# Performance work log

Hardware: AMD Instinct MI355X
Metric: run time of the kernel (lower is better)

Reference implementation:

```python
import jax, jax.numpy as jnp
import numpy as np
from jax import lax

NUM_CLASSES = 2
PATCH_NUM = 4
TEMP = 0.5
THRESHOLD = 0.6
BDP, FDP = 0.1, 0.9
W_CONTR, W_ENT, W_CONS = 0.1, 0.01, 1.0
RAMP = 40
EPOCH_SEMI = 5
IGNORE = 255


def conv(x, w, stride):
    return lax.conv_general_dilated(x, w, (stride, stride), 'SAME',
                                    dimension_numbers=('NCHW', 'OIHW', 'NCHW'))


def extractor(x, W1, W2, W3):
    h = jax.nn.relu(conv(x, W1, 2))
    h = jax.nn.relu(conv(h, W2, 2))
    return jax.nn.relu(conv(h, W3, 2))  # stride-8 features [B,256,H/8,W/8]


def resize_bilinear_ac(x, oh, ow):
    # bilinear, align_corners=True (matches F.interpolate(..., align_corners=True))
    B, C, H, W = x.shape
    ys = jnp.linspace(0.0, H - 1.0, oh)
    xs = jnp.linspace(0.0, W - 1.0, ow)
    y0 = jnp.floor(ys).astype(jnp.int32); x0 = jnp.floor(xs).astype(jnp.int32)
    y1 = jnp.minimum(y0 + 1, H - 1);      x1 = jnp.minimum(x0 + 1, W - 1)
    wy = (ys - y0)[:, None].astype(x.dtype)
    wx = (xs - x0)[None, :].astype(x.dtype)
    v00 = x[:, :, y0[:, None], x0[None, :]]
    v01 = x[:, :, y0[:, None], x1[None, :]]
    v10 = x[:, :, y1[:, None], x0[None, :]]
    v11 = x[:, :, y1[:, None], x1[None, :]]
    top = v00 * (1 - wx) + v01 * wx
    bot = v10 * (1 - wx) + v11 * wx
    return top * (1 - wy) + bot * wy


def ce_loss(logits, labels, extra_mask=None):
    # logits [B,C,H,W], labels [B,H,W]; mean over valid pixels
    logp = jax.nn.log_softmax(logits, axis=1)
    safe = jnp.clip(labels, 0, logits.shape[1] - 1)
    nll = -jnp.take_along_axis(logp, safe[:, None], axis=1)[:, 0]
    valid = labels != IGNORE
    if extra_mask is not None:
        valid = valid & extra_mask
    valid = valid.astype(logits.dtype)
    return (nll * valid).sum() / jnp.maximum(valid.sum(), 1.0)


def reference(x_l, y_l, x_ul, epoch, proj_ul_ema, z_ul_ema, W1, W2, W3, Wc, bc, Wp):
    # ---- supervised branch ----
    fea_l = extractor(x_l, W1, W2, W3)
    zl_small = conv(fea_l, Wc, 1) + bc[None, :, None, None]
    z_l = resize_bilinear_ac(zl_small, x_l.shape[2], x_l.shape[3])
    loss_sup = ce_loss(z_l, y_l)
    if epoch < EPOCH_SEMI:
        return loss_sup

    # ---- unsupervised branch ----
    fea_ul = extractor(x_ul, W1, W2, W3)
    proj_ul = conv(fea_ul, Wp, 1)
    proj_ul = proj_ul / jnp.maximum(
        jnp.linalg.norm(proj_ul, axis=1, keepdims=True), 1e-12)
    z_ul = conv(fea_ul, Wc, 1) + bc[None, :, None, None]

    # entropy minimization
    logp_ul = jax.nn.log_softmax(z_ul, axis=1)
    p_ul = jnp.exp(logp_ul)
    loss_ent = (-(p_ul * logp_ul).sum(axis=1)).mean()

    pseudo_label = jnp.argmax(z_ul, axis=1)
    p_ema = jax.nn.softmax(z_ul_ema, axis=1)
    max_probs_ema = p_ema.max(axis=1)
    pseudo_label_ema = jnp.argmax(z_ul_ema, axis=1)
    mask_confident = max_probs_ema > THRESHOLD
    loss_cons = ce_loss(z_ul, pseudo_label_ema, mask_confident)

    # ---- vectorized patch extraction (replaces python loops) ----
    B, C, Hp, Wp_ = proj_ul.shape
    P = PATCH_NUM
    h, w = Hp // P, Wp_ // P

    def to_patches(t):  # [B,C,Hp,Wp] -> [P*P*B, h*w, C], torch loop order (j,k,ii)
        return t.reshape(B, C, P, h, P, w).transpose(2, 4, 0, 3, 5, 1).reshape(P * P * B, h * w, C)

    def lab_patches(l):  # [B,Hp,Wp] -> [P*P*B, h*w]
        return l.reshape(B, P, h, P, w).transpose(1, 3, 0, 2, 4).reshape(P * P * B, h * w)

    pat_s = to_patches(proj_ul)
    pat_e = to_patches(proj_ul_ema)
    lab_s = lab_patches(pseudo_label)
    lab_e = lab_patches(pseudo_label_ema)

    feat_all = jnp.concatenate([pat_s.reshape(-1, C), pat_e.reshape(-1, C)], axis=0)  # [M,C]
    lab_all = jnp.concatenate([lab_s.reshape(-1), lab_e.reshape(-1)], axis=0)

    fc = lab_s.astype(proj_ul.dtype).mean(axis=1)  # foreground fraction per patch
    include = jnp.logical_not((fc > BDP) & (fc < FDP)).astype(proj_ul.dtype)

    def patch_loss(anchors, labels_i):  # anchors [hw,C]
        logits = (anchors @ feat_all.T) / TEMP        # [hw, M]
        logp = jax.nn.log_softmax(logits, axis=-1)
        pos = (labels_i[:, None] == lab_all[None, :]).astype(logits.dtype)
        per_anchor = -(pos * logp).sum(-1) / jnp.maximum(pos.sum(-1), 1.0)
        return per_anchor.mean()

    losses = jax.vmap(patch_loss)(pat_s, lab_s)       # [P*P*B]
    loss_contr = (losses * include).sum() / jnp.maximum(include.sum(), 1.0)

    ramp = min(max(epoch / RAMP, 0.0), 1.0)
    cons_w = W_CONS * float(np.exp(-5.0 * (1.0 - ramp) ** 2))

    loss_tot = loss_sup + W_CONTR * loss_contr + cons_w * loss_cons + W_ENT * loss_ent
    return loss_tot


def setup_inputs() -> dict:
    key = jax.random.key(0)
    ks = jax.random.split(key, 12)
    s = 0.05
    return {
        'x_l': jax.random.normal(ks[0], (4, 3, 320, 320), jnp.float32),
        'y_l': jax.random.randint(ks[1], (4, 320, 320), 0, NUM_CLASSES),
        'x_ul': jax.random.normal(ks[2], (4, 3, 320, 320), jnp.float32),
        'epoch': 10,
        'proj_ul_ema': jax.random.normal(ks[3], (4, 128, 40, 40), jnp.float32),
        'z_ul_ema': jax.random.normal(ks[4], (4, 2, 40, 40), jnp.float32),
        'W1': jax.random.normal(ks[5], (64, 3, 3, 3), jnp.float32) * s,
        'W2': jax.random.normal(ks[6], (128, 64, 3, 3), jnp.float32) * s,
        'W3': jax.random.normal(ks[7], (256, 128, 3, 3), jnp.float32) * s,
        'Wc': jax.random.normal(ks[8], (NUM_CLASSES, 256, 1, 1), jnp.float32) * s,
        'bc': jnp.zeros((NUM_CLASSES,), jnp.float32),
        'Wp': jax.random.normal(ks[9], (128, 256, 1, 1), jnp.float32) * s,
    }
```

## Files before the change

kernel.cpp:

```cpp
#include <hip/hip_runtime.h>
#include <math.h>

typedef unsigned short u16;
typedef __attribute__((ext_vector_type(8))) short bf16x8;
typedef __attribute__((ext_vector_type(4))) float f32x4;

static const size_t WS_FEA1B = 0;
static const size_t WS_FEA2B = 6553600;
static const size_t WS_FEA3  = 9830400;
static const size_t WS_ZLS   = 13107200;
static const size_t WS_ZUL   = 13120000;
static const size_t WS_FEATB = 13132800;
static const size_t WS_LAB   = 13952000;
static const size_t WS_PART  = 13964800;
static const size_t WS_ACC   = 14194176;
static const size_t WS_FC    = 14194192;
static const size_t WS_CSUM  = 14194256;
static const size_t WS_WT2   = 14194512;
static const size_t WS_WT3   = 14231376;
static const size_t WS_WPT   = 14378832;

#define NJS 25

__device__ inline u16 f2bf(float x) {
    unsigned int u = __float_as_uint(x);
    unsigned int r = u + 0x7fffu + ((u >> 16) & 1u);
    return (u16)(r >> 16);
}

__global__ __launch_bounds__(256) void wtrans(
    const float* __restrict__ W2, const float* __restrict__ W3,
    const float* __restrict__ Wp,
    u16* __restrict__ wt2, u16* __restrict__ wt3, u16* __restrict__ wpt)
{
    int tid = blockIdx.x * 256 + threadIdx.x;
    if (tid < 73728) {
        int ci = tid & 63, rest = tid >> 6;
        int co = rest & 127, tap = rest >> 7;
        wt2[tid] = f2bf(W2[((size_t)co*64 + ci)*9 + tap]);
    } else if (tid < 368640) {
        int t3 = tid - 73728;
        int ci = t3 & 127, rest = t3 >> 7;
        int co = rest & 255, tap = rest >> 8;
        wt3[t3] = f2bf(W3[((size_t)co*128 + ci)*9 + tap]);
    } else {
        int tp = tid - 368640;
        wpt[tp] = f2bf(Wp[tp]);
    }
}

__global__ __launch_bounds__(256) void conv1_k(
    const float* __restrict__ x_l, const float* __restrict__ x_ul,
    const float* __restrict__ W1, u16* __restrict__ fea1b)
{
    int oy = blockIdx.x;
    int n  = blockIdx.y;
    const float* x = (n < 4) ? x_l + (size_t)n*307200
                             : x_ul + (size_t)(n-4)*307200;
    int t = threadIdx.x;
    int co = t & 63, g = t >> 6;
    __shared__ float lds[9*324];
    for (int u = t; u < 9*322; u += 256) {
        int plane = u / 322, col = u - plane*322;
        int ci = plane / 3, ky = plane - ci*3;
        int iy = oy*2 + ky;
        float v = 0.f;
        if (iy < 320 && col < 320)
            v = x[((size_t)ci*320 + iy)*320 + col];
        lds[plane*324 + col] = v;
    }
    __syncthreads();
    float w[27];
    #pragma unroll
    for (int k = 0; k < 27; ++k) w[k] = W1[co*27 + k];
    float acc[40];
    #pragma unroll
    for (int i = 0; i < 40; ++i) acc[i] = 0.f;
    #pragma unroll
    for (int ci = 0; ci < 3; ++ci) {
        #pragma unroll
        for (int ky = 0; ky < 3; ++ky) {
            const float* base = &lds[(ci*3+ky)*324 + g*80];
            const float* wk = &w[(ci*3+ky)*3];
            #pragma unroll
            for (int q = 0; q < 10; ++q) {
                float4 a = *(const float4*)&base[q*8];
                float4 b = *(const float4*)&base[q*8+4];
                float2 c = *(const float2*)&base[q*8+8];
                float xx[10] = {a.x,a.y,a.z,a.w,b.x,b.y,b.z,b.w,c.x,c.y};
                #pragma unroll
                for (int oo = 0; oo < 4; ++oo)
                    acc[q*4+oo] += wk[0]*xx[2*oo] + wk[1]*xx[2*oo+1] + wk[2]*xx[2*oo+2];
            }
        }
    }
    u16* dst = fea1b + (((size_t)n*160 + oy)*160 + g*40)*64 + co;
    #pragma unroll
    for (int i = 0; i < 40; ++i)
        dst[(size_t)i*64] = f2bf(fmaxf(acc[i], 0.f));
}

template<int Ci, int Co, int H, int OH, int COG, bool OB>
__global__ __launch_bounds__(256) void conv3x3_nhwc(
    const u16* __restrict__ inb, const u16* __restrict__ wt,
    u16* __restrict__ outb, float* __restrict__ outf)
{
    constexpr int TILES = OH/8;
    int tile = blockIdx.x;
    int co0  = blockIdx.y * (64*COG);
    int n    = blockIdx.z;
    int ty = tile / TILES, tx = tile - ty*TILES;
    int oy0 = ty*8, ox0 = tx*8;
    int iy0 = oy0*2, ix0 = ox0*2;
    int t = threadIdx.x, lane = t & 63, wv = t >> 6;
    int idx15 = lane & 15, kg = lane >> 4;

    __shared__ u16 lds[306*40];

    f32x4 acc[COG][4];
    #pragma unroll
    for (int cog = 0; cog < COG; ++cog)
        #pragma unroll
        for (int nt = 0; nt < 4; ++nt) acc[cog][nt] = (f32x4){0.f,0.f,0.f,0.f};

    int goff[5], loff[5];
    #pragma unroll
    for (int i = 0; i < 5; ++i) {
        int u = t + i*256;
        if (u < 1224) {
            int pix = u >> 2, q = u & 3;
            int iyl = pix / 18, j = pix - iyl*18;
            int iy = iy0 + iyl, ix = ix0 + j;
            bool ok = (iy < H && ix < H);
            goff[i] = ok ? (((n*H + iy)*H + ix)*Ci + q*8) : -1;
            int jp = (j & 1)*9 + (j >> 1);
            loff[i] = (iyl*18 + jp)*40 + q*8;
        } else goff[i] = -2;
    }
    uint4 vreg[5];
    #pragma unroll
    for (int i = 0; i < 5; ++i) {
        if (goff[i] == -2) continue;
        vreg[i] = (goff[i] >= 0) ? *(const uint4*)&inb[(size_t)goff[i]]
                                 : make_uint4(0,0,0,0);
    }

    for (int c0 = 0; c0 < Ci; c0 += 32) {
        __syncthreads();
        #pragma unroll
        for (int i = 0; i < 5; ++i)
            if (goff[i] != -2) *(uint4*)&lds[loff[i]] = vreg[i];
        __syncthreads();
        if (c0 + 32 < Ci) {
            #pragma unroll
            for (int i = 0; i < 5; ++i) {
                if (goff[i] == -2) continue;
                vreg[i] = (goff[i] >= 0) ? *(const uint4*)&inb[(size_t)goff[i] + c0 + 32]
                                         : make_uint4(0,0,0,0);
            }
        }

        bf16x8 A[COG][9];
        #pragma unroll
        for (int cog = 0; cog < COG; ++cog) {
            const u16* wb = wt + (size_t)(co0 + cog*64 + wv*16 + idx15)*Ci + c0 + kg*8;
            #pragma unroll
            for (int tap = 0; tap < 9; ++tap)
                A[cog][tap] = *(const bf16x8*)(wb + (size_t)tap*Co*Ci);
        }

        #pragma unroll
        for (int tap = 0; tap < 9; ++tap) {
            int ky = tap/3, kx = tap - ky*3;
            #pragma unroll
            for (int nt = 0; nt < 4; ++nt) {
                int l = nt*16 + idx15;
                int iyl = 2*(l>>3) + ky;
                int j = 2*(l&7) + kx;
                int jp = (j&1)*9 + (j>>1);
                bf16x8 B = *(const bf16x8*)&lds[(size_t)(iyl*18 + jp)*40 + kg*8];
                #pragma unroll
                for (int cog = 0; cog < COG; ++cog)
                    acc[cog][nt] = __builtin_amdgcn_mfma_f32_16x16x32_bf16(A[cog][tap], B, acc[cog][nt], 0, 0, 0);
            }
        }
    }

    #pragma unroll
    for (int cog = 0; cog < COG; ++cog) {
        int co = co0 + cog*64 + wv*16 + kg*4;
        #pragma unroll
        for (int nt = 0; nt < 4; ++nt) {
            int l = nt*16 + idx15;
            int oy = oy0 + (l>>3), ox = ox0 + (l&7);
            if (OB) {
                u16* dst = outb + (((size_t)n*OH + oy)*OH + ox)*Co + co;
                unsigned int p0 = (unsigned int)f2bf(fmaxf(acc[cog][nt][0],0.f))
                                | ((unsigned int)f2bf(fmaxf(acc[cog][nt][1],0.f)) << 16);
                unsigned int p1 = (unsigned int)f2bf(fmaxf(acc[cog][nt][2],0.f))
                                | ((unsigned int)f2bf(fmaxf(acc[cog][nt][3],0.f)) << 16);
                *(uint2*)dst = make_uint2(p0, p1);
            } else {
                #pragma unroll
                for (int r = 0; r < 4; ++r)
                    outf[(((size_t)n*Co + co + r)*OH + oy)*OH + ox] = fmaxf(acc[cog][nt][r], 0.f);
            }
        }
    }
}

__global__ __launch_bounds__(256) void conv1x1_cls(
    const float* __restrict__ fea, const float* __restrict__ Wc,
    float* __restrict__ z)
{
    int idx = blockIdx.x * 256 + threadIdx.x;
    int cc0 = blockIdx.y * 32;
    int n = idx / 1600, r = idx - n*1600;
    const float* f = fea + ((size_t)n*256 + cc0)*1600 + r;
    float a0 = 0.f, a1 = 0.f;
    #pragma unroll
    for (int ci = 0; ci < 32; ++ci) {
        float v = f[(size_t)ci*1600];
        a0 += v * Wc[cc0+ci];
        a1 += v * Wc[256+cc0+ci];
    }
    atomicAdd(&z[(size_t)n*3200 + r], a0);
    atomicAdd(&z[(size_t)n*3200 + 1600 + r], a1);
}

__global__ __launch_bounds__(256) void loss_sup_kernel(
    const float* __restrict__ zs, const int* __restrict__ y,
    const float* __restrict__ bc, float* __restrict__ acc)
{
    const float step = 39.0f / 319.0f;
    float b0 = bc[0], b1 = bc[1];
    float vn = 0.f, vd = 0.f;
    for (int idx = blockIdx.x*256 + threadIdx.x; idx < 409600; idx += gridDim.x*256) {
        int n  = idx / 102400;
        int r  = idx - n*102400;
        int oy = r / 320, ox = r - oy*320;
        float ty = (float)oy * step, tx = (float)ox * step;
        int y0 = (int)ty, x0 = (int)tx;
        int y1 = min(y0 + 1, 39), x1 = min(x0 + 1, 39);
        float wy = ty - (float)y0, wx = tx - (float)x0;
        const float* base = zs + (size_t)n * 3200;
        float z[2];
        #pragma unroll
        for (int c = 0; c < 2; ++c) {
            const float* pl = base + c * 1600;
            float v00 = pl[y0*40 + x0], v01 = pl[y0*40 + x1];
            float v10 = pl[y1*40 + x0], v11 = pl[y1*40 + x1];
            float top = v00 * (1.f - wx) + v01 * wx;
            float bot = v10 * (1.f - wx) + v11 * wx;
            z[c] = top * (1.f - wy) + bot * wy + (c ? b1 : b0);
        }
        int lab = y[idx];
        bool valid = (lab != 255);
        int sl = min(max(lab, 0), 1);
        float mz  = fmaxf(z[0], z[1]);
        float lse = mz + logf(expf(z[0]-mz) + expf(z[1]-mz));
        float nll = lse - z[sl];
        if (valid) { vn += nll; vd += 1.f; }
    }
    #pragma unroll
    for (int off = 32; off; off >>= 1) { vn += __shfl_down(vn, off); vd += __shfl_down(vd, off); }
    __shared__ float rb[8];
    int wv = threadIdx.x >> 6;
    if ((threadIdx.x & 63) == 0) { rb[wv*2] = vn; rb[wv*2+1] = vd; }
    __syncthreads();
    if (threadIdx.x == 0) {
        atomicAdd(&acc[0], rb[0]+rb[2]+rb[4]+rb[6]);
        atomicAdd(&acc[1], rb[1]+rb[3]+rb[5]+rb[7]);
    }
}

__global__ __launch_bounds__(256) void ul_small_kernel(
    const float* __restrict__ z_ul, const float* __restrict__ z_ema,
    const float* __restrict__ bc,
    int* __restrict__ lab_all, float* __restrict__ acc, float* __restrict__ fc_cnt)
{
    int idx = blockIdx.x * 256 + threadIdx.x;
    int n = idx / 1600;
    int r = idx - n*1600;
    int yy = r / 40, xx = r - yy*40;
    float z0 = z_ul[(size_t)n*3200 + r] + bc[0];
    float z1 = z_ul[(size_t)n*3200 + 1600 + r] + bc[1];
    float m = fmaxf(z0, z1);
    float e0 = expf(z0 - m), e1 = expf(z1 - m);
    float lse = m + logf(e0 + e1);
    float lp0 = z0 - lse, lp1 = z1 - lse;
    float p0 = expf(lp0), p1 = expf(lp1);
    float ent = -(p0*lp0 + p1*lp1);
    int pl = (z1 > z0) ? 1 : 0;
    float ze0 = z_ema[(size_t)n*3200 + r], ze1 = z_ema[(size_t)n*3200 + 1600 + r];
    float me = fmaxf(ze0, ze1);
    float f0 = expf(ze0 - me), f1 = expf(ze1 - me);
    float maxp = 1.f / (f0 + f1);
    int ple = (ze1 > ze0) ? 1 : 0;
    bool mask = (maxp > 0.6f);
    float nll = lse - (ple ? z1 : z0);

    int pi = yy / 10, hi = yy % 10, pj = xx / 10, wi = xx % 10;
    int patch = (pi*4 + pj)*4 + n;
    int row = patch * 100 + hi*10 + wi;
    lab_all[row]        = pl;
    lab_all[6400 + row] = ple;
    atomicAdd(&fc_cnt[patch], (float)pl);

    float cn = mask ? nll : 0.f;
    float cd = mask ? 1.f : 0.f;
    #pragma unroll
    for (int off = 32; off; off >>= 1) {
        ent += __shfl_down(ent, off);
        cn  += __shfl_down(cn, off);
        cd  += __shfl_down(cd, off);
    }
    if ((threadIdx.x & 63) == 0) {
        atomicAdd(&acc[2], ent);
        atomicAdd(&acc[3], cn);
        atomicAdd(&acc[4], cd);
    }
}

__global__ __launch_bounds__(256) void proj_mfma(
    const float* __restrict__ fea, const u16* __restrict__ wpt,
    u16* __restrict__ feat)
{
    __shared__ unsigned int lds[128*16];
    __shared__ float nrm[4][16];
    int b = blockIdx.x;
    int n = b / 100;
    int r0 = (b - n*100) * 16;
    int t = threadIdx.x, lane = t & 63, wv = t >> 6;
    int idx15 = lane & 15, kg = lane >> 4;

    const float* fb = fea + (size_t)n * 256 * 1600 + r0;
    #pragma unroll
    for (int i = 0; i < 2; ++i) {
        int flat = i*256 + t;
        int px4 = flat & 3, cp = flat >> 2;
        float4 v0 = *(const float4*)&fb[(size_t)(2*cp)*1600 + px4*4];
        float4 v1 = *(const float4*)&fb[(size_t)(2*cp+1)*1600 + px4*4];
        int s = (cp >> 1) & 3;
        float a0[4] = {v0.x, v0.y, v0.z, v0.w};
        float a1[4] = {v1.x, v1.y, v1.z, v1.w};
        #pragma unroll
        for (int j = 0; j < 4; ++j) {
            unsigned int pk = (unsigned int)f2bf(a0[j]) | ((unsigned int)f2bf(a1[j]) << 16);
            lds[cp*16 + ((px4*4 + j) ^ s)] = pk;
        }
    }

    bf16x8 A[2][8];
    #pragma unroll
    for (int mi = 0; mi < 2; ++mi) {
        const u16* wrow = wpt + (size_t)(wv*32 + mi*16 + idx15)*256 + kg*8;
        #pragma unroll
        for (int ks = 0; ks < 8; ++ks)
            A[mi][ks] = *(const bf16x8*)(wrow + ks*32);
    }
    __syncthreads();

    f32x4 acc[2];
    acc[0] = (f32x4){0.f,0.f,0.f,0.f};
    acc[1] = (f32x4){0.f,0.f,0.f,0.f};

    #pragma unroll
    for (int ks = 0; ks < 8; ++ks) {
        union { unsigned int u[4]; bf16x8 v; } bw;
        #pragma unroll
        for (int w = 0; w < 4; ++w) {
            int cp = ks*16 + kg*4 + w;
            int s = (cp >> 1) & 3;
            bw.u[w] = lds[cp*16 + (idx15 ^ s)];
        }
        acc[0] = __builtin_amdgcn_mfma_f32_16x16x32_bf16(A[0][ks], bw.v, acc[0], 0, 0, 0);
        acc[1] = __builtin_amdgcn_mfma_f32_16x16x32_bf16(A[1][ks], bw.v, acc[1], 0, 0, 0);
    }

    float sq = 0.f;
    #pragma unroll
    for (int mi = 0; mi < 2; ++mi)
        #pragma unroll
        for (int r = 0; r < 4; ++r) sq += acc[mi][r]*acc[mi][r];
    sq += __shfl_xor(sq, 16);
    sq += __shfl_xor(sq, 32);
    if (kg == 0) nrm[wv][idx15] = sq;
    __syncthreads();

    float tot = nrm[0][idx15] + nrm[1][idx15] + nrm[2][idx15] + nrm[3][idx15];
    float scale = 1.f / fmaxf(sqrtf(tot), 1e-12f);
    int rr = r0 + idx15;
    int yy = rr / 40, xx = rr - yy*40;
    int row = ((yy/10*4 + xx/10)*4 + n)*100 + (yy%10)*10 + (xx%10);
    unsigned int* dst = (unsigned int*)(feat + (size_t)row*128) + wv*16 + kg*2;
    #pragma unroll
    for (int mi = 0; mi < 2; ++mi) {
        #pragma unroll
        for (int pr = 0; pr < 2; ++pr) {
            unsigned int pk = (unsigned int)f2bf(acc[mi][2*pr]*scale)
                            | ((unsigned int)f2bf(acc[mi][2*pr+1]*scale) << 16);
            dst[mi*8 + pr] = pk;
        }
    }
}

__global__ __launch_bounds__(256) void ema_scatter(
    const float* __restrict__ ema, u16* __restrict__ feat,
    unsigned int* __restrict__ maxn)
{
    __shared__ float lds[128*64];
    int b = blockIdx.x;
    int n = b / 25;
    int r0 = (b - n*25) * 64;
    int t = threadIdx.x, lane = t & 63, wv = t >> 6;

    const float* src = ema + ((size_t)n*128 + wv*32)*1600 + r0 + lane;
    int scol = lane ^ (wv << 3);
    #pragma unroll
    for (int cc = 0; cc < 32; ++cc)
        lds[(wv*32 + cc)*64 + scol] = src[(size_t)cc*1600];
    __syncthreads();

    int pxl = t >> 2, cq = t & 3;
    int r = r0 + pxl;
    int yy = r / 40, xx = r - yy*40;
    int row = 6400 + ((yy/10*4 + xx/10)*4 + n)*100 + (yy%10)*10 + (xx%10);
    int rcol = pxl ^ (cq << 3);
    float sq = 0.f;
    unsigned int pk[16];
    #pragma unroll
    for (int i = 0; i < 16; ++i) {
        float v0 = lds[(cq*32 + 2*i)*64 + rcol];
        float v1 = lds[(cq*32 + 2*i + 1)*64 + rcol];
        sq += v0*v0 + v1*v1;
        pk[i] = (unsigned int)f2bf(v0) | ((unsigned int)f2bf(v1) << 16);
    }
    u16* dst = feat + (size_t)row*128 + cq*32;
    #pragma unroll
    for (int i = 0; i < 4; ++i)
        *(uint4*)&((unsigned int*)dst)[i*4] = *(uint4*)&pk[i*4];

    sq += __shfl_xor(sq, 1);
    sq += __shfl_xor(sq, 2);
    float mx = sq;
    #pragma unroll
    for (int off = 4; off < 64; off <<= 1) mx = fmaxf(mx, __shfl_xor(mx, off));
    __shared__ float red[4];
    if (lane == 0) red[wv] = mx;
    __syncthreads();
    if (t == 0)
        atomicMax(maxn, __float_as_uint(fmaxf(fmaxf(red[0], red[1]),
                                              fmaxf(red[2], red[3]))));
}

__global__ __launch_bounds__(256) void class_sum(
    const u16* __restrict__ feat, const int* __restrict__ lab,
    float* __restrict__ csum, float* __restrict__ acc)
{
    int t = threadIdx.x;
    int chp = t & 63;
    int s   = t >> 6;
    int r0 = blockIdx.x * 400;
    float s00=0.f, s01=0.f, s10=0.f, s11=0.f;
    float c1 = 0.f;
    for (int i = s; i < 400; i += 4) {
        int row = r0 + i;
        unsigned int pk = ((const unsigned int*)feat)[(size_t)row*64 + chp];
        float v0 = __uint_as_float(pk << 16);
        float v1 = __uint_as_float(pk & 0xffff0000u);
        int la = lab[row];
        if (la) { s10 += v0; s11 += v1; }
        else    { s00 += v0; s01 += v1; }
        if (chp == 0) c1 += (float)la;
    }
    __shared__ float red[4][256];
    __shared__ float cbuf[4];
    red[s][chp*4+0] = s00; red[s][chp*4+1] = s01;
    red[s][chp*4+2] = s10; red[s][chp*4+3] = s11;
    if (chp == 0) cbuf[s] = c1;
    __syncthreads();
    if (s == 0) {
        #pragma unroll
        for (int k = 0; k < 4; ++k) {
            float v = red[0][chp*4+k] + red[1][chp*4+k] + red[2][chp*4+k] + red[3][chp*4+k];
            int cls = k >> 1, par = k & 1;
            atomicAdd(&csum[cls*128 + 2*chp + par], v);
        }
    }
    if (t == 0)
        atomicAdd(&acc[8], cbuf[0]+cbuf[1]+cbuf[2]+cbuf[3]);
}

__global__ __launch_bounds__(256) void contrast_sE(
    const u16* __restrict__ feat, const unsigned int* __restrict__ maxn,
    float* __restrict__ partials)
{
    int js = blockIdx.x;
    int p  = blockIdx.y;
    int t = threadIdx.x, lane = t & 63, wv = t >> 6;
    int idx15 = lane & 15;
    int kg = lane >> 4;

    __shared__ u16 lds[2][32*128];

    float M = 2.f * sqrtf(__uint_as_float(*maxn)) + 4.f;
    float M2 = M * 1.44269504f;

    bf16x8 A[2][4];
    bf16x8 zz = {0,0,0,0,0,0,0,0};
    #pragma unroll
    for (int mi = 0; mi < 2; ++mi) {
        int m = wv + mi*4;
        #pragma unroll
        for (int c = 0; c < 4; ++c) {
            int a = 16*m + idx15;
            A[mi][c] = (m < 7 && a < 100)
                ? *(const bf16x8*)&feat[(size_t)(p*100 + a)*128 + c*32 + kg*8]
                : zz;
        }
    }

    int jbase = js * 512;
    float sE[8] = {};

    int row0 = t >> 4, row1 = 16 + row0;
    int gin  = t & 15;
    int off0 = row0*128 + ((gin ^ row0) << 3);
    int off1 = row1*128 + ((gin ^ (row1 & 15)) << 3);
    const u16* sbase = feat + (size_t)jbase*128 + t*8;

    uint4 v0 = *(const uint4*)(sbase);
    uint4 v1 = *(const uint4*)(sbase + 2048);
    *(uint4*)&lds[0][off0] = v0;
    *(uint4*)&lds[0][off1] = v1;
    __syncthreads();

    for (int ch = 0; ch < 16; ++ch) {
        int cur = ch & 1;
        if (ch < 15) {
            v0 = *(const uint4*)(sbase + (size_t)(ch+1)*4096);
            v1 = *(const uint4*)(sbase + (size_t)(ch+1)*4096 + 2048);
        }

        #pragma unroll
        for (int nt = 0; nt < 2; ++nt) {
            int r = nt*16 + idx15;
            bf16x8 B[4];
            #pragma unroll
            for (int c = 0; c < 4; ++c) {
                int gs = (c*4 + kg) ^ (r & 15);
                B[c] = *(const bf16x8*)&lds[cur][r*128 + gs*8];
            }
            #pragma unroll
            for (int mi = 0; mi < 2; ++mi) {
                int m = wv + mi*4;
                if (m < 7) {
                    f32x4 C = {0.f, 0.f, 0.f, 0.f};
                    #pragma unroll
                    for (int c = 0; c < 4; ++c)
                        C = __builtin_amdgcn_mfma_f32_16x16x32_bf16(A[mi][c], B[c], C, 0, 0, 0);
                    #pragma unroll
                    for (int rr = 0; rr < 4; ++rr)
                        sE[mi*4+rr] += __builtin_amdgcn_exp2f(C[rr] * 2.885390082f - M2);
                }
            }
        }

        if (ch < 15) {
            *(uint4*)&lds[cur^1][off0] = v0;
            *(uint4*)&lds[cur^1][off1] = v1;
        }
        __syncthreads();
    }

    #pragma unroll
    for (int mi = 0; mi < 2; ++mi) {
        int m = wv + mi*4;
        if (m < 7) {
            #pragma unroll
            for (int r = 0; r < 4; ++r) {
                float s = sE[mi*4+r];
                #pragma unroll
                for (int off = 1; off < 16; off <<= 1)
                    s += __shfl_xor(s, off);
                if (idx15 == 0) {
                    int a = 16*m + 4*kg + r;
                    partials[((size_t)p*NJS + js)*112 + a] = s;
                }
            }
        }
    }
}

__global__ __launch_bounds__(128) void merge_contrast(
    const float* __restrict__ partials, const float* __restrict__ fc_cnt,
    const unsigned int* __restrict__ maxn, const u16* __restrict__ feat,
    const int* __restrict__ lab, const float* __restrict__ csum,
    float* __restrict__ acc)
{
    int p = blockIdx.x, t = threadIdx.x;
    float pa = 0.f;
    if (t < 100) {
        float s = 0.f;
        for (int js = 0; js < NJS; ++js)
            s += partials[((size_t)p*NJS + js)*112 + t];
        int row = p*100 + t;
        int la = lab[row];
        const float* Sv = csum + la*128;
        const unsigned int* av = (const unsigned int*)(feat + (size_t)row*128);
        float dp = 0.f;
        #pragma unroll
        for (int i = 0; i < 64; ++i) {
            unsigned int pk = av[i];
            dp += __uint_as_float(pk << 16) * Sv[2*i]
                + __uint_as_float(pk & 0xffff0000u) * Sv[2*i+1];
        }
        float N1 = acc[8];
        float cnt = la ? N1 : (12800.f - N1);
        float M = 2.f * sqrtf(__uint_as_float(*maxn)) + 4.f;
        pa = M + logf(s) - 2.f * dp / fmaxf(cnt, 1.f);
    }
    #pragma unroll
    for (int off = 32; off; off >>= 1) pa += __shfl_down(pa, off);
    __shared__ float w2[2];
    if ((t & 63) == 0) w2[t >> 6] = pa;
    __syncthreads();
    if (t == 0) {
        float loss_p = (w2[0] + w2[1]) / 100.f;
        float fcv = fc_cnt[p] / 100.f;
        float inc = ((fcv > 0.1f) && (fcv < 0.9f)) ? 0.f : 1.f;
        atomicAdd(&acc[5], loss_p * inc);
        atomicAdd(&acc[6], inc);
    }
}

__global__ void final_kernel(const float* __restrict__ acc,
                             const int* __restrict__ epoch_p,
                             float* __restrict__ out)
{
    if (threadIdx.x == 0 && blockIdx.x == 0) {
        float loss_sup = acc[0] / fmaxf(acc[1], 1.f);
        int epoch = *epoch_p;
        float loss = loss_sup;
        if (epoch >= 5) {
            float contr = acc[5] / fmaxf(acc[6], 1.f);
            float cons  = acc[3] / fmaxf(acc[4], 1.f);
            float ent   = acc[2] / 6400.f;
            float ramp  = fminf(fmaxf((float)epoch / 40.f, 0.f), 1.f);
            float d = 1.f - ramp;
            float cons_w = expf(-5.f * d * d);
            loss = loss_sup + 0.1f * contr + cons_w * cons + 0.01f * ent;
        }
        out[0] = loss;
    }
}

extern "C" void kernel_launch(void* const* d_in, const int* in_sizes, int n_in,
                              void* d_out, int out_size, void* d_ws, size_t ws_size,
                              hipStream_t stream)
{
    const float* x_l      = (const float*)d_in[0];
    const int*   y_l      = (const int*)  d_in[1];
    const float* x_ul     = (const float*)d_in[2];
    const int*   epoch    = (const int*)  d_in[3];
    const float* proj_ema = (const float*)d_in[4];
    const float* z_ema    = (const float*)d_in[5];
    const float* W1       = (const float*)d_in[6];
    const float* W2       = (const float*)d_in[7];
    const float* W3       = (const float*)d_in[8];
    const float* Wc       = (const float*)d_in[9];
    const float* bc       = (const float*)d_in[10];
    const float* Wp       = (const float*)d_in[11];
    float* out = (float*)d_out;
    float* ws  = (float*)d_ws;

    u16*   fea1b = (u16*)(ws + WS_FEA1B);
    u16*   fea2b = (u16*)(ws + WS_FEA2B);
    float* fea3  = ws + WS_FEA3;
    float* zls   = ws + WS_ZLS;
    float* zul   = ws + WS_ZUL;
    u16*   featB = (u16*)(ws + WS_FEATB);
    int*   labA  = (int*)(ws + WS_LAB);
    float* part  = ws + WS_PART;
    float* acc   = ws + WS_ACC;
    float* fc    = ws + WS_FC;
    float* csum  = ws + WS_CSUM;
    u16*   wt2   = (u16*)(ws + WS_WT2);
    u16*   wt3   = (u16*)(ws + WS_WT3);
    u16*   wpt   = (u16*)(ws + WS_WPT);
    unsigned int* maxn = (unsigned int*)(acc + 7);

    hipMemsetAsync(acc, 0, 336 * sizeof(float), stream);
    hipMemsetAsync(zls, 0, 25600 * sizeof(float), stream);

    wtrans<<<1568, 256, 0, stream>>>(W2, W3, Wp, wt2, wt3, wpt);

    conv1_k<<<dim3(160, 8), 256, 0, stream>>>(x_l, x_ul, W1, fea1b);
    conv3x3_nhwc<64,128,160,80,2,true><<<dim3(100, 1, 8), 256, 0, stream>>>(fea1b, wt2, fea2b, nullptr);
    conv3x3_nhwc<128,256,80,40,2,false><<<dim3(25, 2, 8), 256, 0, stream>>>(fea2b, wt3, nullptr, fea3);
    conv1x1_cls<<<dim3(50, 8), 256, 0, stream>>>(fea3, Wc, zls);

    loss_sup_kernel<<<512, 256, 0, stream>>>(zls, y_l, bc, acc);
    ul_small_kernel<<<25, 256, 0, stream>>>(zul, z_ema, bc, labA, acc, fc);

    proj_mfma<<<400, 256, 0, stream>>>(fea3 + 4*409600, wpt, featB);
    ema_scatter<<<100, 256, 0, stream>>>(proj_ema, featB, maxn);
    class_sum<<<32, 256, 0, stream>>>(featB, labA, csum, acc);

    contrast_sE<<<dim3(NJS, 64), 256, 0, stream>>>(featB, maxn, part);
    merge_contrast<<<64, 128, 0, stream>>>(part, fc, maxn, featB, labA, csum, acc);
    final_kernel<<<1, 64, 0, stream>>>(acc, epoch, out);
}
```

Before: 216.5 us.

## Store stride-8 features in bf16 NHWC and tile feat layout for direct MFMA loads

The third conv now writes bf16 NHWC instead of fp32 NCHW. The classifier 1x1 conv reads it with vector loads and drops the atomics and the memset, and the projection kernel feeds MFMA straight from global memory with no LDS transpose. The contrast feature matrix moves to a 16-row tiled layout, so the contrast kernel loads B fragments directly from global without LDS double buffering. Each contrast block now handles two anchor patches to reuse the loaded B tiles, which halves the grid. The classifier input is now bf16 instead of fp32, so it loses some precision.

```diff
diff --git a/kernel.cpp b/kernel.cpp
--- a/kernel.cpp
+++ b/kernel.cpp
@@ -7,25 +7,29 @@
 
 static const size_t WS_FEA1B = 0;
 static const size_t WS_FEA2B = 6553600;
-static const size_t WS_FEA3  = 9830400;
-static const size_t WS_ZLS   = 13107200;
-static const size_t WS_ZUL   = 13120000;
-static const size_t WS_FEATB = 13132800;
-static const size_t WS_LAB   = 13952000;
-static const size_t WS_PART  = 13964800;
-static const size_t WS_ACC   = 14194176;
-static const size_t WS_FC    = 14194192;
-static const size_t WS_CSUM  = 14194256;
-static const size_t WS_WT2   = 14194512;
-static const size_t WS_WT3   = 14231376;
-static const size_t WS_WPT   = 14378832;
+static const size_t WS_FEA3B = 9830400;
+static const size_t WS_ZLS   = 11468800;
+static const size_t WS_ZUL   = 11481600;
+static const size_t WS_FEATT = 11494400;
+static const size_t WS_LAB   = 13132800;
+static const size_t WS_PART  = 13145600;
+static const size_t WS_ACC   = 13324800;
+static const size_t WS_FC    = 13324816;
+static const size_t WS_CSUM  = 13324880;
+static const size_t WS_WT2   = 13325136;
+static const size_t WS_WT3   = 13362000;
+static const size_t WS_WPT   = 13509456;
 
 #define NJS 25
+
 
 __device__ inline u16 f2bf(float x) {
     unsigned int u = __float_as_uint(x);
     unsigned int r = u + 0x7fffu + ((u >> 16) & 1u);
     return (u16)(r >> 16);
+}
+__device__ inline float bf2f(u16 v) {
+    return __uint_as_float((unsigned int)v << 16);
 }
 
 __global__ __launch_bounds__(256) void wtrans(
@@ -100,10 +104,10 @@
         dst[(size_t)i*64] = f2bf(fmaxf(acc[i], 0.f));
 }
 
-template<int Ci, int Co, int H, int OH, int COG, bool OB>
+template<int Ci, int Co, int H, int OH, int COG>
 __global__ __launch_bounds__(256) void conv3x3_nhwc(
     const u16* __restrict__ inb, const u16* __restrict__ wt,
-    u16* __restrict__ outb, float* __restrict__ outf)
+    u16* __restrict__ outb)
 {
     constexpr int TILES = OH/8;
     int tile = blockIdx.x;
@@ -193,39 +197,36 @@
         for (int nt = 0; nt < 4; ++nt) {
             int l = nt*16 + idx15;
             int oy = oy0 + (l>>3), ox = ox0 + (l&7);
-            if (OB) {
-                u16* dst = outb + (((size_t)n*OH + oy)*OH + ox)*Co + co;
-                unsigned int p0 = (unsigned int)f2bf(fmaxf(acc[cog][nt][0],0.f))
-                                | ((unsigned int)f2bf(fmaxf(acc[cog][nt][1],0.f)) << 16);
-                unsigned int p1 = (unsigned int)f2bf(fmaxf(acc[cog][nt][2],0.f))
-                                | ((unsigned int)f2bf(fmaxf(acc[cog][nt][3],0.f)) << 16);
-                *(uint2*)dst = make_uint2(p0, p1);
-            } else {
-                #pragma unroll
-                for (int r = 0; r < 4; ++r)
-                    outf[(((size_t)n*Co + co + r)*OH + oy)*OH + ox] = fmaxf(acc[cog][nt][r], 0.f);
-            }
+            u16* dst = outb + (((size_t)n*OH + oy)*OH + ox)*Co + co;
+            unsigned int p0 = (unsigned int)f2bf(fmaxf(acc[cog][nt][0],0.f))
+                            | ((unsigned int)f2bf(fmaxf(acc[cog][nt][1],0.f)) << 16);
+            unsigned int p1 = (unsigned int)f2bf(fmaxf(acc[cog][nt][2],0.f))
+                            | ((unsigned int)f2bf(fmaxf(acc[cog][nt][3],0.f)) << 16);
+            *(uint2*)dst = make_uint2(p0, p1);
         }
     }
 }
 
 __global__ __launch_bounds__(256) void conv1x1_cls(
-    const float* __restrict__ fea, const float* __restrict__ Wc,
+    const u16* __restrict__ feab, const float* __restrict__ Wc,
     float* __restrict__ z)
 {
     int idx = blockIdx.x * 256 + threadIdx.x;
-    int cc0 = blockIdx.y * 32;
     int n = idx / 1600, r = idx - n*1600;
-    const float* f = fea + ((size_t)n*256 + cc0)*1600 + r;
+    const u16* f = feab + (size_t)idx * 256;
     float a0 = 0.f, a1 = 0.f;
     #pragma unroll
-    for (int ci = 0; ci < 32; ++ci) {
-        float v = f[(size_t)ci*1600];
-        a0 += v * Wc[cc0+ci];
-        a1 += v * Wc[256+cc0+ci];
-    }
-    atomicAdd(&z[(size_t)n*3200 + r], a0);
-    atomicAdd(&z[(size_t)n*3200 + 1600 + r], a1);
+    for (int ci = 0; ci < 256; ci += 8) {
+        bf16x8 v = *(const bf16x8*)&f[ci];
+        #pragma unroll
+        for (int j = 0; j < 8; ++j) {
+            float x = bf2f((u16)v[j]);
+            a0 += x * Wc[ci+j];
+            a1 += x * Wc[256+ci+j];
+        }
+    }
+    z[(size_t)n*3200 + r]        = a0;
+    z[(size_t)n*3200 + 1600 + r] = a1;
 }
 
 __global__ __launch_bounds__(256) void loss_sup_kernel(
@@ -323,33 +324,17 @@
 }
 
 __global__ __launch_bounds__(256) void proj_mfma(
-    const float* __restrict__ fea, const u16* __restrict__ wpt,
-    u16* __restrict__ feat)
-{
-    __shared__ unsigned int lds[128*16];
+    const u16* __restrict__ fea3b, const u16* __restrict__ wpt,
+    u16* __restrict__ featT)
+{
     __shared__ float nrm[4][16];
     int b = blockIdx.x;
     int n = b / 100;
-    int r0 = (b - n*100) * 16;
+    int px0 = (b - n*100) * 16;
     int t = threadIdx.x, lane = t & 63, wv = t >> 6;
     int idx15 = lane & 15, kg = lane >> 4;
 
-    const float* fb = fea + (size_t)n * 256 * 1600 + r0;
-    #pragma unroll
-    for (int i = 0; i < 2; ++i) {
-        int flat = i*256 + t;
-        int px4 = flat & 3, cp = flat >> 2;
-        float4 v0 = *(const float4*)&fb[(size_t)(2*cp)*1600 + px4*4];
-        float4 v1 = *(const float4*)&fb[(size_t)(2*cp+1)*1600 + px4*4];
-        int s = (cp >> 1) & 3;
-        float a0[4] = {v0.x, v0.y, v0.z, v0.w};
-        float a1[4] = {v1.x, v1.y, v1.z, v1.w};
-        #pragma unroll
-        for (int j = 0; j < 4; ++j) {
-            unsigned int pk = (unsigned int)f2bf(a0[j]) | ((unsigned int)f2bf(a1[j]) << 16);
-            lds[cp*16 + ((px4*4 + j) ^ s)] = pk;
-        }
-    }
+    const u16* fb = fea3b + ((size_t)(4+n)*1600 + px0) * 256;
 
     bf16x8 A[2][8];
     #pragma unroll
@@ -359,7 +344,6 @@
         for (int ks = 0; ks < 8; ++ks)
             A[mi][ks] = *(const bf16x8*)(wrow + ks*32);
     }
-    __syncthreads();
 
     f32x4 acc[2];
     acc[0] = (f32x4){0.f,0.f,0.f,0.f};
@@ -367,15 +351,9 @@
 
     #pragma unroll
     for (int ks = 0; ks < 8; ++ks) {
-        union { unsigned int u[4]; bf16x8 v; } bw;
-        #pragma unroll
-        for (int w = 0; w < 4; ++w) {
-            int cp = ks*16 + kg*4 + w;
-            int s = (cp >> 1) & 3;
-            bw.u[w] = lds[cp*16 + (idx15 ^ s)];
-        }
-        acc[0] = __builtin_amdgcn_mfma_f32_16x16x32_bf16(A[0][ks], bw.v, acc[0], 0, 0, 0);
-        acc[1] = __builtin_amdgcn_mfma_f32_16x16x32_bf16(A[1][ks], bw.v, acc[1], 0, 0, 0);
+        bf16x8 B = *(const bf16x8*)&fb[(size_t)idx15*256 + ks*32 + kg*8];
+        acc[0] = __builtin_amdgcn_mfma_f32_16x16x32_bf16(A[0][ks], B, acc[0], 0, 0, 0);
+        acc[1] = __builtin_amdgcn_mfma_f32_16x16x32_bf16(A[1][ks], B, acc[1], 0, 0, 0);
     }
 
     float sq = 0.f;
@@ -390,23 +368,26 @@
 
     float tot = nrm[0][idx15] + nrm[1][idx15] + nrm[2][idx15] + nrm[3][idx15];
     float scale = 1.f / fmaxf(sqrtf(tot), 1e-12f);
-    int rr = r0 + idx15;
+    int rr = px0 + idx15;
     int yy = rr / 40, xx = rr - yy*40;
     int row = ((yy/10*4 + xx/10)*4 + n)*100 + (yy%10)*10 + (xx%10);
-    unsigned int* dst = (unsigned int*)(feat + (size_t)row*128) + wv*16 + kg*2;
+    int jt = row >> 4, rl = row & 15;
+    u16* base = featT + (size_t)jt*4096 + rl*16;
     #pragma unroll
     for (int mi = 0; mi < 2; ++mi) {
         #pragma unroll
         for (int pr = 0; pr < 2; ++pr) {
             unsigned int pk = (unsigned int)f2bf(acc[mi][2*pr]*scale)
                             | ((unsigned int)f2bf(acc[mi][2*pr+1]*scale) << 16);
-            dst[mi*8 + pr] = pk;
+            int q = kg*4 + 2*pr;
+            int g = wv*4 + mi*2 + (q >> 3);
+            *(unsigned int*)&base[g*256 + (q & 7)] = pk;
         }
     }
 }
 
 __global__ __launch_bounds__(256) void ema_scatter(
-    const float* __restrict__ ema, u16* __restrict__ feat,
+    const float* __restrict__ ema, u16* __restrict__ featT,
     unsigned int* __restrict__ maxn)
 {
     __shared__ float lds[128*64];
@@ -436,10 +417,13 @@
         sq += v0*v0 + v1*v1;
         pk[i] = (unsigned int)f2bf(v0) | ((unsigned int)f2bf(v1) << 16);
     }
-    u16* dst = feat + (size_t)row*128 + cq*32;
-    #pragma unroll
-    for (int i = 0; i < 4; ++i)
-        *(uint4*)&((unsigned int*)dst)[i*4] = *(uint4*)&pk[i*4];
+    int jt = row >> 4, rl = row & 15;
+    u16* base = featT + (size_t)jt*4096 + rl*16;
+    #pragma unroll
+    for (int k8 = 0; k8 < 4; ++k8) {
+        int g = cq*4 + k8;
+        *(uint4*)&base[g*256] = *(uint4*)&pk[k8*4];
+    }
 
     sq += __shfl_xor(sq, 1);
     sq += __shfl_xor(sq, 2);
@@ -455,18 +439,20 @@
 }
 
 __global__ __launch_bounds__(256) void class_sum(
-    const u16* __restrict__ feat, const int* __restrict__ lab,
+    const u16* __restrict__ featT, const int* __restrict__ lab,
     float* __restrict__ csum, float* __restrict__ acc)
 {
     int t = threadIdx.x;
     int chp = t & 63;
     int s   = t >> 6;
     int r0 = blockIdx.x * 400;
+    int g = chp >> 2, go = (chp & 3) * 2;
     float s00=0.f, s01=0.f, s10=0.f, s11=0.f;
     float c1 = 0.f;
     for (int i = s; i < 400; i += 4) {
         int row = r0 + i;
-        unsigned int pk = ((const unsigned int*)feat)[(size_t)row*64 + chp];
+        int jt = row >> 4, rl = row & 15;
+        unsigned int pk = *(const unsigned int*)&featT[(size_t)jt*4096 + g*256 + rl*16 + go];
         float v0 = __uint_as_float(pk << 16);
         float v1 = __uint_as_float(pk & 0xffff0000u);
         int la = lab[row];
@@ -493,65 +479,49 @@
 }
 
 __global__ __launch_bounds__(256) void contrast_sE(
-    const u16* __restrict__ feat, const unsigned int* __restrict__ maxn,
+    const u16* __restrict__ featT, const unsigned int* __restrict__ maxn,
     float* __restrict__ partials)
 {
     int js = blockIdx.x;
-    int p  = blockIdx.y;
+    int p0 = blockIdx.y * 2;
     int t = threadIdx.x, lane = t & 63, wv = t >> 6;
     int idx15 = lane & 15;
     int kg = lane >> 4;
 
-    __shared__ u16 lds[2][32*128];
-
     float M = 2.f * sqrtf(__uint_as_float(*maxn)) + 4.f;
     float M2 = M * 1.44269504f;
 
-    bf16x8 A[2][4];
+    bf16x8 A[2][2][4];
     bf16x8 zz = {0,0,0,0,0,0,0,0};
     #pragma unroll
-    for (int mi = 0; mi < 2; ++mi) {
-        int m = wv + mi*4;
-        #pragma unroll
-        for (int c = 0; c < 4; ++c) {
-            int a = 16*m + idx15;
-            A[mi][c] = (m < 7 && a < 100)
-                ? *(const bf16x8*)&feat[(size_t)(p*100 + a)*128 + c*32 + kg*8]
-                : zz;
-        }
-    }
-
-    int jbase = js * 512;
-    float sE[8] = {};
-
-    int row0 = t >> 4, row1 = 16 + row0;
-    int gin  = t & 15;
-    int off0 = row0*128 + ((gin ^ row0) << 3);
-    int off1 = row1*128 + ((gin ^ (row1 & 15)) << 3);
-    const u16* sbase = feat + (size_t)jbase*128 + t*8;
-
-    uint4 v0 = *(const uint4*)(sbase);
-    uint4 v1 = *(const uint4*)(sbase + 2048);
-    *(uint4*)&lds[0][off0] = v0;
-    *(uint4*)&lds[0][off1] = v1;
-    __syncthreads();
-
-    for (int ch = 0; ch < 16; ++ch) {
-        int cur = ch & 1;
-        if (ch < 15) {
-            v0 = *(const uint4*)(sbase + (size_t)(ch+1)*4096);
-            v1 = *(const uint4*)(sbase + (size_t)(ch+1)*4096 + 2048);
-        }
-
-        #pragma unroll
-        for (int nt = 0; nt < 2; ++nt) {
-            int r = nt*16 + idx15;
-            bf16x8 B[4];
+    for (int pi = 0; pi < 2; ++pi) {
+        #pragma unroll
+        for (int mi = 0; mi < 2; ++mi) {
+            int m = wv + mi*4;
             #pragma unroll
             for (int c = 0; c < 4; ++c) {
-                int gs = (c*4 + kg) ^ (r & 15);
-                B[c] = *(const bf16x8*)&lds[cur][r*128 + gs*8];
+                int a = 16*m + idx15;
+                if (m < 7 && a < 100) {
+                    int row = (p0+pi)*100 + a;
+                    A[pi][mi][c] = *(const bf16x8*)&featT[
+                        (size_t)(row >> 4)*4096 + (c*4 + kg)*256 + (row & 15)*16];
+                } else A[pi][mi][c] = zz;
             }
+        }
+    }
+
+    float sE[2][8] = {};
+    const u16* jb = featT + (size_t)(js*32)*4096 + (size_t)kg*256 + (size_t)idx15*16;
+
+    #pragma unroll 2
+    for (int jt = 0; jt < 32; ++jt) {
+        bf16x8 B[4];
+        #pragma unroll
+        for (int c = 0; c < 4; ++c)
+            B[c] = *(const bf16x8*)(jb + (size_t)jt*4096 + c*1024);
+
+        #pragma unroll
+        for (int pi = 0; pi < 2; ++pi) {
             #pragma unroll
             for (int mi = 0; mi < 2; ++mi) {
                 int m = wv + mi*4;
@@ -559,34 +529,31 @@
                     f32x4 C = {0.f, 0.f, 0.f, 0.f};
                     #pragma unroll
                     for (int c = 0; c < 4; ++c)
-                        C = __builtin_amdgcn_mfma_f32_16x16x32_bf16(A[mi][c], B[c], C, 0, 0, 0);
+                        C = __builtin_amdgcn_mfma_f32_16x16x32_bf16(A[pi][mi][c], B[c], C, 0, 0, 0);
                     #pragma unroll
                     for (int rr = 0; rr < 4; ++rr)
-                        sE[mi*4+rr] += __builtin_amdgcn_exp2f(C[rr] * 2.885390082f - M2);
+                        sE[pi][mi*4+rr] += __builtin_amdgcn_exp2f(C[rr] * 2.885390082f - M2);
                 }
             }
         }
-
-        if (ch < 15) {
-            *(uint4*)&lds[cur^1][off0] = v0;
-            *(uint4*)&lds[cur^1][off1] = v1;
-        }
-        __syncthreads();
-    }
-
-    #pragma unroll
-    for (int mi = 0; mi < 2; ++mi) {
-        int m = wv + mi*4;
-        if (m < 7) {
-            #pragma unroll
-            for (int r = 0; r < 4; ++r) {
-                float s = sE[mi*4+r];
+    }
+
+    #pragma unroll
+    for (int pi = 0; pi < 2; ++pi) {
+        #pragma unroll
+        for (int mi = 0; mi < 2; ++mi) {
+            int m = wv + mi*4;
+            if (m < 7) {
                 #pragma unroll
-                for (int off = 1; off < 16; off <<= 1)
-                    s += __shfl_xor(s, off);
-                if (idx15 == 0) {
-                    int a = 16*m + 4*kg + r;
-                    partials[((size_t)p*NJS + js)*112 + a] = s;
+                for (int r = 0; r < 4; ++r) {
+                    float s = sE[pi][mi*4+r];
+                    #pragma unroll
+                    for (int off = 1; off < 16; off <<= 1)
+                        s += __shfl_xor(s, off);
+                    if (idx15 == 0) {
+                        int a = 16*m + 4*kg + r;
+                        partials[((size_t)(p0+pi)*NJS + js)*112 + a] = s;
+                    }
                 }
             }
         }
@@ -595,7 +562,7 @@
 
 __global__ __launch_bounds__(128) void merge_contrast(
     const float* __restrict__ partials, const float* __restrict__ fc_cnt,
-    const unsigned int* __restrict__ maxn, const u16* __restrict__ feat,
+    const unsigned int* __restrict__ maxn, const u16* __restrict__ featT,
     const int* __restrict__ lab, const float* __restrict__ csum,
     float* __restrict__ acc)
 {
@@ -608,11 +575,12 @@
         int row = p*100 + t;
         int la = lab[row];
         const float* Sv = csum + la*128;
-        const unsigned int* av = (const unsigned int*)(feat + (size_t)row*128);
+        int jt = row >> 4, rl = row & 15;
+        const u16* base = featT + (size_t)jt*4096 + rl*16;
         float dp = 0.f;
         #pragma unroll
         for (int i = 0; i < 64; ++i) {
-            unsigned int pk = av[i];
+            unsigned int pk = *(const unsigned int*)&base[(i >> 2)*256 + (i & 3)*2];
             dp += __uint_as_float(pk << 16) * Sv[2*i]
                 + __uint_as_float(pk & 0xffff0000u) * Sv[2*i+1];
         }
@@ -677,10 +645,10 @@
 
     u16*   fea1b = (u16*)(ws + WS_FEA1B);
     u16*   fea2b = (u16*)(ws + WS_FEA2B);
-    float* fea3  = ws + WS_FEA3;
+    u16*   fea3b = (u16*)(ws + WS_FEA3B);
     float* zls   = ws + WS_ZLS;
     float* zul   = ws + WS_ZUL;
-    u16*   featB = (u16*)(ws + WS_FEATB);
+    u16*   featT = (u16*)(ws + WS_FEATT);
     int*   labA  = (int*)(ws + WS_LAB);
     float* part  = ws + WS_PART;
     float* acc   = ws + WS_ACC;
@@ -692,23 +660,22 @@
     unsigned int* maxn = (unsigned int*)(acc + 7);
 
     hipMemsetAsync(acc, 0, 336 * sizeof(float), stream);
-    hipMemsetAsync(zls, 0, 25600 * sizeof(float), stream);
 
     wtrans<<<1568, 256, 0, stream>>>(W2, W3, Wp, wt2, wt3, wpt);
 
     conv1_k<<<dim3(160, 8), 256, 0, stream>>>(x_l, x_ul, W1, fea1b);
-    conv3x3_nhwc<64,128,160,80,2,true><<<dim3(100, 1, 8), 256, 0, stream>>>(fea1b, wt2, fea2b, nullptr);
-    conv3x3_nhwc<128,256,80,40,2,false><<<dim3(25, 2, 8), 256, 0, stream>>>(fea2b, wt3, nullptr, fea3);
-    conv1x1_cls<<<dim3(50, 8), 256, 0, stream>>>(fea3, Wc, zls);
+    conv3x3_nhwc<64,128,160,80,2><<<dim3(100, 1, 8), 256, 0, stream>>>(fea1b, wt2, fea2b);
+    conv3x3_nhwc<128,256,80,40,2><<<dim3(25, 2, 8), 256, 0, stream>>>(fea2b, wt3, fea3b);
+    conv1x1_cls<<<50, 256, 0, stream>>>(fea3b, Wc, zls);
 
     loss_sup_kernel<<<512, 256, 0, stream>>>(zls, y_l, bc, acc);
     ul_small_kernel<<<25, 256, 0, stream>>>(zul, z_ema, bc, labA, acc, fc);
 
-    proj_mfma<<<400, 256, 0, stream>>>(fea3 + 4*409600, wpt, featB);
-    ema_scatter<<<100, 256, 0, stream>>>(proj_ema, featB, maxn);
-    class_sum<<<32, 256, 0, stream>>>(featB, labA, csum, acc);
-
-    contrast_sE<<<dim3(NJS, 64), 256, 0, stream>>>(featB, maxn, part);
-    merge_contrast<<<64, 128, 0, stream>>>(part, fc, maxn, featB, labA, csum, acc);
+    proj_mfma<<<400, 256, 0, stream>>>(fea3b, wpt, featT);
+    ema_scatter<<<100, 256, 0, stream>>>(proj_ema, featT, maxn);
+    class_sum<<<32, 256, 0, stream>>>(featT, labA, csum, acc);
+
+    contrast_sE<<<dim3(NJS, 32), 256, 0, stream>>>(featT, maxn, part);
+    merge_contrast<<<64, 128, 0, stream>>>(part, fc, maxn, featT, labA, csum, acc);
     final_kernel<<<1, 64, 0, stream>>>(acc, epoch, out);
 }
```

Result: slower. 225.3 us (+4.1%).
